# Kernel tuning notes

Measured on AMD Instinct MI355X. Metric: run time of the kernel, lower is better.

Reference implementation:

```python
import jax, jax.numpy as jnp
import numpy as np

T, B, C, H = 2048, 4, 1024, 16
DK = C // H
CLAMP = 1e8  # fp32 clamp bound used by the original module


def setup_inputs() -> dict:
    key = jax.random.key(0)
    ks = jax.random.split(key, 12)
    s = 1.0 / np.sqrt(C)
    inp = {
        'query': jax.random.normal(ks[0], (T, B, C), jnp.float32),
        'key': jax.random.normal(ks[1], (T, B, C), jnp.float32),
        'value': jax.random.normal(ks[2], (T, B, C), jnp.float32),
        'key_padding_mask': jax.random.randint(ks[3], (B, T), 0, 2) > 0,
        # nn.Linear params, stored torch-style as [out, in]
        'Wq': jax.random.uniform(ks[4], (C, C), jnp.float32, -s, s),
        'bq': jax.random.uniform(ks[5], (C,), jnp.float32, -s, s),
        'Wk': jax.random.uniform(ks[6], (C, C), jnp.float32, -s, s),
        'bk': jax.random.uniform(ks[7], (C,), jnp.float32, -s, s),
        'Wv': jax.random.uniform(ks[8], (C, C), jnp.float32, -s, s),
        'bv': jax.random.uniform(ks[9], (C,), jnp.float32, -s, s),
        'Wo': jax.random.uniform(ks[10], (C, C), jnp.float32, -s, s),
        'bo': jax.random.uniform(ks[11], (C,), jnp.float32, -s, s),
    }
    return inp


def _attn(query, key, value, key_padding_mask, Wq, bq, Wk, bk, Wv, bv, Wo, bo):
    # T x B x C -> B x T x C
    q_in = jnp.swapaxes(query, 0, 1)
    k_in = jnp.swapaxes(key, 0, 1)
    v_in = jnp.swapaxes(value, 0, 1)
    b = q_in.shape[0]
    # projections (torch Linear: x @ W.T + b), split heads -> B x H x T x dk
    q = (q_in @ Wq.T + bq).reshape(b, -1, H, DK).transpose(0, 2, 1, 3)
    k = (k_in @ Wk.T + bk).reshape(b, -1, H, DK).transpose(0, 2, 1, 3)
    v = (v_in @ Wv.T + bv).reshape(b, -1, H, DK).transpose(0, 2, 1, 3)
    scores = jnp.einsum('bhqd,bhkd->bhqk', q, k) / np.sqrt(DK)
    if key_padding_mask is not None:
        scores = jnp.where(key_padding_mask[:, None, None, :], -jnp.inf, scores)
    scores = jnp.clip(scores, -CLAMP, CLAMP)
    attn = jax.nn.softmax(scores.astype(jnp.float32), axis=-1).astype(scores.dtype)
    # dropout is identity in eval mode
    x = jnp.einsum('bhqk,bhkd->bhqd', attn, v)
    x = x.transpose(0, 2, 1, 3).reshape(b, -1, H * DK)
    out = x @ Wo.T + bo
    return jnp.swapaxes(out, 0, 1)  # back to T x B x C


def reference(query, key, value, key_padding_mask, Wq, bq, Wk, bk, Wv, bv, Wo, bo):
    return _attn(query, key, value, key_padding_mask, Wq, bq, Wk, bk, Wv, bv, Wo, bo)
```

## Files before the change

### kernel.cpp

```cpp
#include <hip/hip_runtime.h>
#include <hip/hip_bf16.h>
#include <cstddef>
#include <cstdint>

constexpr int T  = 2048;
constexpr int B  = 4;
constexpr int C  = 1024;
constexpr int H  = 16;
constexpr int DK = 64;
constexpr int M  = T * B;
constexpr int NT = T / 64;

typedef __attribute__((ext_vector_type(8))) short bf16x8;
typedef __attribute__((ext_vector_type(4))) float f32x4;
typedef __attribute__((ext_vector_type(4))) unsigned short u16x4;
typedef __attribute__((ext_vector_type(8))) unsigned short u16x8;

__device__ inline unsigned short f2bf(float f) {
    union { float f; uint32_t u; } v; v.f = f;
    uint32_t u = v.u + 0x7fff + ((v.u >> 16) & 1);
    return (unsigned short)(u >> 16);
}
__device__ inline float bf2f(unsigned short h) {
    union { uint32_t u; float f; } v; v.u = (uint32_t)h << 16;
    return v.f;
}
__device__ inline uint32_t cvtpk_bf16(float lo, float hi) {
    uint32_t r;
    asm("v_cvt_pk_bf16_f32 %0, %1, %2" : "=v"(r) : "v"(lo), "v"(hi));
    return r;
}
__device__ inline void cfence() { asm volatile("" ::: "memory"); }

__device__ inline void block_sync_lds() {
    __builtin_amdgcn_sched_barrier(0);
    asm volatile("s_waitcnt lgkmcnt(0)" ::: "memory");
    __builtin_amdgcn_sched_barrier(0);
    __builtin_amdgcn_s_barrier();
    __builtin_amdgcn_sched_barrier(0);
}

__device__ inline void gload_lds16(const void* g, void* l) {
    auto gp = reinterpret_cast<const __attribute__((address_space(1))) char*>(
        reinterpret_cast<uintptr_t>(g));
    auto lp = reinterpret_cast<__attribute__((address_space(3))) char*>(
        reinterpret_cast<uintptr_t>(l));
    __builtin_amdgcn_global_load_lds(gp, lp, 16, 0, 0);
}

__global__ __launch_bounds__(256) void convert_in(const float* __restrict__ q,
                                                  const float* __restrict__ k,
                                                  const float* __restrict__ v,
                                                  unsigned short* __restrict__ dq,
                                                  unsigned short* __restrict__ dk2,
                                                  unsigned short* __restrict__ dv) {
    const float* s; unsigned short* d;
    if (blockIdx.y == 0) { s = q; d = dq; }
    else if (blockIdx.y == 1) { s = k; d = dk2; }
    else { s = v; d = dv; }
    const size_t i = ((size_t)blockIdx.x * 256 + threadIdx.x) * 8;
    const float4 a = *(const float4*)(s + i);
    const float4 b = *(const float4*)(s + i + 4);
    u16x8 o;
    o[0] = f2bf(a.x); o[1] = f2bf(a.y); o[2] = f2bf(a.z); o[3] = f2bf(a.w);
    o[4] = f2bf(b.x); o[5] = f2bf(b.y); o[6] = f2bf(b.z); o[7] = f2bf(b.w);
    *(u16x8*)(d + i) = o;
}

__global__ __launch_bounds__(256) void convert_w(const float* __restrict__ wq,
                                                 const float* __restrict__ wk,
                                                 const float* __restrict__ wv,
                                                 unsigned short* __restrict__ dst) {
    const float* s = blockIdx.y == 0 ? wq : (blockIdx.y == 1 ? wk : wv);
    unsigned short* d = dst + (size_t)blockIdx.y * C * C;
    const size_t i = ((size_t)blockIdx.x * 256 + threadIdx.x) * 8;
    const float4 a = *(const float4*)(s + i);
    const float4 b = *(const float4*)(s + i + 4);
    u16x8 o;
    o[0] = f2bf(a.x); o[1] = f2bf(a.y); o[2] = f2bf(a.z); o[3] = f2bf(a.w);
    o[4] = f2bf(b.x); o[5] = f2bf(b.y); o[6] = f2bf(b.z); o[7] = f2bf(b.w);
    *(u16x8*)(d + i) = o;
}

__global__ __launch_bounds__(256) void convert_wo(const float* __restrict__ wo,
                                                  unsigned short* __restrict__ hi,
                                                  unsigned short* __restrict__ lo) {
    const size_t i = ((size_t)blockIdx.x * 256 + threadIdx.x) * 8;
#pragma unroll
    for (int j = 0; j < 8; j++) {
        const float x = wo[i + j];
        const unsigned short h = f2bf(x);
        hi[i + j] = h;
        lo[i + j] = f2bf(x - bf2f(h));
    }
}

__global__ __launch_bounds__(256) void qkv_gemm(
        const unsigned short* __restrict__ Aq,
        const unsigned short* __restrict__ Ak,
        const unsigned short* __restrict__ Av,
        const unsigned short* __restrict__ W,
        const float* __restrict__ bq, const float* __restrict__ bk,
        const float* __restrict__ bv,
        unsigned short* __restrict__ Qb, unsigned short* __restrict__ Kb,
        unsigned short* __restrict__ Vb) {
    __shared__ __align__(16) unsigned short As[128][32];
    __shared__ __align__(16) unsigned short Ws[128][32];

    const int tid = threadIdx.x;
    const int m0 = blockIdx.x * 128;
    const int n0 = blockIdx.y * 128;
    const int w = tid >> 6, lane = tid & 63;
    const int g = lane >> 4, c16 = lane & 15;
    const int wr = (w >> 1) * 64, wc = (w & 1) * 64;

    const int which = n0 >> 10;
    const unsigned short* A = which == 0 ? Aq : (which == 1 ? Ak : Av);

    f32x4 acc[4][4] = {};

    for (int k0 = 0; k0 < C; k0 += 32) {
        __syncthreads();
#pragma unroll
        for (int half = 0; half < 2; half++) {
            const int chunk = tid + half * 256;
            const int r = chunk >> 2, s = chunk & 3;
            gload_lds16(A + (size_t)(m0 + r) * C + k0 + s * 8,
                        (char*)&As[0][0] + chunk * 16);
            gload_lds16(W + (size_t)(n0 + r) * C + k0 + s * 8,
                        (char*)&Ws[0][0] + chunk * 16);
        }
        __syncthreads();

        bf16x8 af[4], bfr[4];
#pragma unroll
        for (int mf = 0; mf < 4; mf++)
            af[mf] = *(const bf16x8*)&As[wr + mf * 16 + c16][g * 8];
#pragma unroll
        for (int nf = 0; nf < 4; nf++)
            bfr[nf] = *(const bf16x8*)&Ws[wc + nf * 16 + c16][g * 8];
#pragma unroll
        for (int mf = 0; mf < 4; mf++)
#pragma unroll
            for (int nf = 0; nf < 4; nf++)
                acc[mf][nf] = __builtin_amdgcn_mfma_f32_16x16x32_bf16(
                    af[mf], bfr[nf], acc[mf][nf], 0, 0, 0);
    }

    unsigned short* dst = which == 0 ? Qb : (which == 1 ? Kb : Vb);
    const float* bias = which == 0 ? bq : (which == 1 ? bk : bv);
    const float scale = which == 0 ? 0.180336889f : 1.0f;

#pragma unroll
    for (int mf = 0; mf < 4; mf++) {
#pragma unroll
        for (int nf = 0; nf < 4; nf++) {
            const int n = n0 + wc + nf * 16 + c16;
            const int c = n & 1023;
            const int hh = c >> 6, dk = c & 63;
            const float bval = bias[c];
#pragma unroll
            for (int r = 0; r < 4; r++) {
                const int m = m0 + wr + mf * 16 + g * 4 + r;
                const int t = m >> 2, bb = m & 3;
                dst[((size_t)(bb * H + hh) * T + t) * DK + dk] =
                    f2bf((acc[mf][nf][r] + bval) * scale);
            }
        }
    }
}

__global__ __launch_bounds__(256) void oproj_gemm(
        const unsigned short* __restrict__ Xh, const unsigned short* __restrict__ Xl,
        const unsigned short* __restrict__ Wh, const unsigned short* __restrict__ Wl,
        const float* __restrict__ bo, float* __restrict__ out) {
    __shared__ __align__(16) unsigned short Ahs[128][32];
    __shared__ __align__(16) unsigned short Als[128][32];
    __shared__ __align__(16) unsigned short Bhs[128][32];
    __shared__ __align__(16) unsigned short Bls[128][32];

    const int tid = threadIdx.x;
    const int m0 = blockIdx.x * 128;
    const int n0 = blockIdx.y * 128;
    const int w = tid >> 6, lane = tid & 63;
    const int g = lane >> 4, c16 = lane & 15;
    const int wr = (w >> 1) * 64, wc = (w & 1) * 64;

    f32x4 acc[4][4] = {};

    for (int k0 = 0; k0 < C; k0 += 32) {
        __syncthreads();
#pragma unroll
        for (int half = 0; half < 2; half++) {
            const int chunk = tid + half * 256;
            const int r = chunk >> 2, s = chunk & 3;
            const size_t goffA = (size_t)(m0 + r) * C + k0 + s * 8;
            const size_t goffB = (size_t)(n0 + r) * C + k0 + s * 8;
            gload_lds16(Xh + goffA, (char*)&Ahs[0][0] + chunk * 16);
            gload_lds16(Xl + goffA, (char*)&Als[0][0] + chunk * 16);
            gload_lds16(Wh + goffB, (char*)&Bhs[0][0] + chunk * 16);
            gload_lds16(Wl + goffB, (char*)&Bls[0][0] + chunk * 16);
        }
        __syncthreads();

        bf16x8 ah[4], al[4];
#pragma unroll
        for (int mf = 0; mf < 4; mf++) {
            ah[mf] = *(const bf16x8*)&Ahs[wr + mf * 16 + c16][g * 8];
            al[mf] = *(const bf16x8*)&Als[wr + mf * 16 + c16][g * 8];
        }
#pragma unroll
        for (int nf = 0; nf < 4; nf++) {
            const bf16x8 wh = *(const bf16x8*)&Bhs[wc + nf * 16 + c16][g * 8];
            const bf16x8 wl = *(const bf16x8*)&Bls[wc + nf * 16 + c16][g * 8];
#pragma unroll
            for (int mf = 0; mf < 4; mf++) {
                acc[mf][nf] = __builtin_amdgcn_mfma_f32_16x16x32_bf16(ah[mf], wh, acc[mf][nf], 0, 0, 0);
                acc[mf][nf] = __builtin_amdgcn_mfma_f32_16x16x32_bf16(al[mf], wh, acc[mf][nf], 0, 0, 0);
                acc[mf][nf] = __builtin_amdgcn_mfma_f32_16x16x32_bf16(ah[mf], wl, acc[mf][nf], 0, 0, 0);
            }
        }
    }

#pragma unroll
    for (int mf = 0; mf < 4; mf++) {
#pragma unroll
        for (int nf = 0; nf < 4; nf++) {
            const int n = n0 + wc + nf * 16 + c16;
            const float bval = bo[n];
#pragma unroll
            for (int r = 0; r < 4; r++) {
                const int m = m0 + wr + mf * 16 + g * 4 + r;
                const int t = m & 2047, bb = m >> 11;
                out[((size_t)t * B + bb) * C + n] = acc[mf][nf][r] + bval;
            }
        }
    }
}

__global__ __launch_bounds__(256) void attn_mfma(const unsigned short* __restrict__ Q,
                                                 const unsigned short* __restrict__ K,
                                                 const unsigned short* __restrict__ V,
                                                 const int* __restrict__ mask,
                                                 unsigned short* __restrict__ Xh,
                                                 unsigned short* __restrict__ Xl) {
    __shared__ __align__(16) short Ks[2][64][72];
    __shared__ __align__(16) short Vt[2][64][72];
    __shared__ __align__(16) short Pl[4][16][72];

    const int b = blockIdx.z, h = blockIdx.y;
    const int q0 = blockIdx.x * 128;
    const int tid = threadIdx.x;
    const int wl = tid >> 6;
    const int lane = tid & 63;
    const int g = lane >> 4;
    const int c16 = lane & 15;

    const size_t bh = (size_t)(b * H + h) * T * DK;
    const unsigned short* Qg = Q + bh;
    const unsigned short* Kg = K + bh;
    const unsigned short* Vg = V + bh;
    const int* mb = mask + b * T;

    bf16x8 qf[2][2];
#pragma unroll
    for (int qs = 0; qs < 2; qs++)
#pragma unroll
        for (int sl = 0; sl < 2; sl++)
            qf[qs][sl] = *(const bf16x8*)(Qg +
                (size_t)(q0 + wl * 32 + qs * 16 + c16) * DK + g * 8 + sl * 32);

    f32x4 o[2][4] = {};
    float lrow[2] = {0.0f, 0.0f};

    const int skr = tid >> 3;
    const int skc = (tid & 7) * 8;
    const int kp = tid & 31, dc = tid >> 5;
    uint4 kra, krb; u16x8 va, vb; int mw;

#define ISSUE(kv0)                                                              \
    do {                                                                        \
        kra = *(const uint4*)(Kg + (size_t)((kv0) + skr) * DK + skc);           \
        krb = *(const uint4*)(Kg + (size_t)((kv0) + skr + 32) * DK + skc);      \
        va  = *(const u16x8*)(Vg + (size_t)((kv0) + 2 * kp) * DK + dc * 8);     \
        vb  = *(const u16x8*)(Vg + (size_t)((kv0) + 2 * kp + 1) * DK + dc * 8); \
        mw  = mb[(kv0) + lane];                                                 \
    } while (0)

    ISSUE(0);

    for (int kt = 0; kt < NT; ++kt) {
        const int buf = kt & 1;

        const unsigned long long mbits = __ballot(mw != 0);
        *(uint4*)&Ks[buf][skr][skc] = kra;
        *(uint4*)&Ks[buf][skr + 32][skc] = krb;
#pragma unroll
        for (int j = 0; j < 8; j++) {
            *(uint32_t*)&Vt[buf][dc * 8 + j][2 * kp] =
                (uint32_t)(unsigned short)va[j] | ((uint32_t)(unsigned short)vb[j] << 16);
        }
        if (kt + 1 < NT) ISSUE((kt + 1) * 64);

        block_sync_lds();

        bf16x8 kf[4][2], vf[4][2];
#pragma unroll
        for (int t = 0; t < 4; t++)
#pragma unroll
            for (int sl = 0; sl < 2; sl++) {
                kf[t][sl] = *(const bf16x8*)&Ks[buf][t * 16 + c16][g * 8 + sl * 32];
                vf[t][sl] = *(const bf16x8*)&Vt[buf][t * 16 + c16][g * 8 + sl * 32];
            }

#pragma unroll
        for (int qs = 0; qs < 2; qs++) {
            f32x4 s4[4];
#pragma unroll
            for (int t = 0; t < 4; t++) {
                f32x4 acc = {0.f, 0.f, 0.f, 0.f};
                acc = __builtin_amdgcn_mfma_f32_16x16x32_bf16(kf[t][0], qf[qs][0], acc, 0, 0, 0);
                acc = __builtin_amdgcn_mfma_f32_16x16x32_bf16(kf[t][1], qf[qs][1], acc, 0, 0, 0);
                s4[t] = acc;
            }

            float rs = 0.0f;
#pragma unroll
            for (int t = 0; t < 4; t++)
#pragma unroll
                for (int r = 0; r < 4; r++) {
                    float p = __builtin_amdgcn_exp2f(s4[t][r]);
                    const int key = 16 * t + 4 * g + r;
                    p = ((mbits >> key) & 1ull) ? 0.0f : p;
                    s4[t][r] = p;
                    rs += p;
                }
            rs += __shfl_xor(rs, 16);
            rs += __shfl_xor(rs, 32);
            lrow[qs] += rs;

            cfence();
#pragma unroll
            for (int t = 0; t < 4; t++)
#pragma unroll
                for (int rr = 0; rr < 2; rr++) {
                    const uint32_t wv = cvtpk_bf16(s4[t][2 * rr], s4[t][2 * rr + 1]);
                    *(uint32_t*)&Pl[wl][c16][16 * t + 4 * g + 2 * rr] = wv;
                }
            cfence();
            bf16x8 pa[2];
            pa[0] = *(const bf16x8*)&Pl[wl][c16][g * 8];
            pa[1] = *(const bf16x8*)&Pl[wl][c16][g * 8 + 32];
            cfence();

#pragma unroll
            for (int td = 0; td < 4; td++) {
                o[qs][td] = __builtin_amdgcn_mfma_f32_16x16x32_bf16(vf[td][0], pa[0], o[qs][td], 0, 0, 0);
                o[qs][td] = __builtin_amdgcn_mfma_f32_16x16x32_bf16(vf[td][1], pa[1], o[qs][td], 0, 0, 0);
            }
        }
    }
#undef ISSUE

#pragma unroll
    for (int qs = 0; qs < 2; qs++) {
        const float inv = 1.0f / lrow[qs];
        const int qq = q0 + wl * 32 + qs * 16 + c16;
#pragma unroll
        for (int td = 0; td < 4; td++) {
            u16x4 hi4, lo4;
#pragma unroll
            for (int r = 0; r < 4; r++) {
                const float val = o[qs][td][r] * inv;
                const unsigned short hv = f2bf(val);
                hi4[r] = hv;
                lo4[r] = f2bf(val - bf2f(hv));
            }
            const size_t idx = ((size_t)b * T + qq) * C + h * DK + td * 16 + 4 * g;
            *(u16x4*)(Xh + idx) = hi4;
            *(u16x4*)(Xl + idx) = lo4;
        }
    }
}

extern "C" void kernel_launch(void* const* d_in, const int* in_sizes, int n_in,
                              void* d_out, int out_size, void* d_ws, size_t ws_size,
                              hipStream_t stream) {
    const float* query = (const float*)d_in[0];
    const float* key   = (const float*)d_in[1];
    const float* value = (const float*)d_in[2];
    const int*   kpm   = (const int*)d_in[3];
    const float* Wq = (const float*)d_in[4];
    const float* bq = (const float*)d_in[5];
    const float* Wk = (const float*)d_in[6];
    const float* bk = (const float*)d_in[7];
    const float* Wv = (const float*)d_in[8];
    const float* bv = (const float*)d_in[9];
    const float* Wo = (const float*)d_in[10];
    const float* bo = (const float*)d_in[11];

    constexpr size_t MB = 1u << 20;
    char* w8 = (char*)d_ws;
    unsigned short* Qa  = (unsigned short*)(w8 + 0 * MB);
    unsigned short* Ka  = (unsigned short*)(w8 + 16 * MB);
    unsigned short* Va  = (unsigned short*)(w8 + 32 * MB);
    unsigned short* WB  = (unsigned short*)(w8 + 48 * MB);
    unsigned short* WoH = (unsigned short*)(w8 + 54 * MB);
    unsigned short* WoL = (unsigned short*)(w8 + 56 * MB);
    unsigned short* Qb  = (unsigned short*)(w8 + 64 * MB);
    unsigned short* Kb  = (unsigned short*)(w8 + 80 * MB);
    unsigned short* Vb  = (unsigned short*)(w8 + 96 * MB);
    unsigned short* XhB = Qa;
    unsigned short* XlB = Ka;

    const dim3 blk(256);

    convert_in<<<dim3(4096, 3), blk, 0, stream>>>(query, key, value, Qa, Ka, Va);
    convert_w<<<dim3(512, 3), blk, 0, stream>>>(Wq, Wk, Wv, WB);
    convert_wo<<<dim3(512, 1), blk, 0, stream>>>(Wo, WoH, WoL);

    qkv_gemm<<<dim3(M / 128, 3 * C / 128), blk, 0, stream>>>(Qa, Ka, Va, WB,
                                                             bq, bk, bv,
                                                             Qb, Kb, Vb);

    attn_mfma<<<dim3(T / 128, H, B), blk, 0, stream>>>(Qb, Kb, Vb, kpm, XhB, XlB);

    oproj_gemm<<<dim3(M / 128, C / 128), blk, 0, stream>>>(XhB, XlB, WoH, WoL,
                                                           bo, (float*)d_out);
}
```

Before: 273.1 us.

## Fuse input bf16 conversion into QKV GEMM and tune attention inner loop

```diff
diff --git a/kernel.cpp b/kernel.cpp
--- a/kernel.cpp
+++ b/kernel.cpp
@@ -46,25 +46,6 @@
     auto lp = reinterpret_cast<__attribute__((address_space(3))) char*>(
         reinterpret_cast<uintptr_t>(l));
     __builtin_amdgcn_global_load_lds(gp, lp, 16, 0, 0);
-}
-
-__global__ __launch_bounds__(256) void convert_in(const float* __restrict__ q,
-                                                  const float* __restrict__ k,
-                                                  const float* __restrict__ v,
-                                                  unsigned short* __restrict__ dq,
-                                                  unsigned short* __restrict__ dk2,
-                                                  unsigned short* __restrict__ dv) {
-    const float* s; unsigned short* d;
-    if (blockIdx.y == 0) { s = q; d = dq; }
-    else if (blockIdx.y == 1) { s = k; d = dk2; }
-    else { s = v; d = dv; }
-    const size_t i = ((size_t)blockIdx.x * 256 + threadIdx.x) * 8;
-    const float4 a = *(const float4*)(s + i);
-    const float4 b = *(const float4*)(s + i + 4);
-    u16x8 o;
-    o[0] = f2bf(a.x); o[1] = f2bf(a.y); o[2] = f2bf(a.z); o[3] = f2bf(a.w);
-    o[4] = f2bf(b.x); o[5] = f2bf(b.y); o[6] = f2bf(b.z); o[7] = f2bf(b.w);
-    *(u16x8*)(d + i) = o;
 }
 
 __global__ __launch_bounds__(256) void convert_w(const float* __restrict__ wq,
@@ -96,9 +77,9 @@
 }
 
 __global__ __launch_bounds__(256) void qkv_gemm(
-        const unsigned short* __restrict__ Aq,
-        const unsigned short* __restrict__ Ak,
-        const unsigned short* __restrict__ Av,
+        const float* __restrict__ Aq,
+        const float* __restrict__ Ak,
+        const float* __restrict__ Av,
         const unsigned short* __restrict__ W,
         const float* __restrict__ bq, const float* __restrict__ bk,
         const float* __restrict__ bv,
@@ -115,7 +96,10 @@
     const int wr = (w >> 1) * 64, wc = (w & 1) * 64;
 
     const int which = n0 >> 10;
-    const unsigned short* A = which == 0 ? Aq : (which == 1 ? Ak : Av);
+    const float* A = which == 0 ? Aq : (which == 1 ? Ak : Av);
+
+    const int ar = tid >> 1;
+    const int ab = (tid & 1) * 16;
 
     f32x4 acc[4][4] = {};
 
@@ -125,10 +109,22 @@
         for (int half = 0; half < 2; half++) {
             const int chunk = tid + half * 256;
             const int r = chunk >> 2, s = chunk & 3;
-            gload_lds16(A + (size_t)(m0 + r) * C + k0 + s * 8,
-                        (char*)&As[0][0] + chunk * 16);
             gload_lds16(W + (size_t)(n0 + r) * C + k0 + s * 8,
                         (char*)&Ws[0][0] + chunk * 16);
+        }
+        {
+            const float* Ap = A + (size_t)(m0 + ar) * C + k0 + ab;
+            const float4 a0 = *(const float4*)(Ap + 0);
+            const float4 a1 = *(const float4*)(Ap + 4);
+            const float4 a2 = *(const float4*)(Ap + 8);
+            const float4 a3 = *(const float4*)(Ap + 12);
+            uint4 w0, w1;
+            w0.x = cvtpk_bf16(a0.x, a0.y); w0.y = cvtpk_bf16(a0.z, a0.w);
+            w0.z = cvtpk_bf16(a1.x, a1.y); w0.w = cvtpk_bf16(a1.z, a1.w);
+            w1.x = cvtpk_bf16(a2.x, a2.y); w1.y = cvtpk_bf16(a2.z, a2.w);
+            w1.z = cvtpk_bf16(a3.x, a3.y); w1.w = cvtpk_bf16(a3.z, a3.w);
+            *(uint4*)&As[ar][ab] = w0;
+            *(uint4*)&As[ar][ab + 8] = w1;
         }
         __syncthreads();
 
@@ -304,6 +300,10 @@
 
         block_sync_lds();
 
+        const unsigned long long nib = mbits >> (4 * g);
+        const uint32_t nlo = (uint32_t)nib;
+        const uint32_t nhi = (uint32_t)(nib >> 32);
+
         bf16x8 kf[4][2], vf[4][2];
 #pragma unroll
         for (int t = 0; t < 4; t++)
@@ -316,6 +316,7 @@
 #pragma unroll
         for (int qs = 0; qs < 2; qs++) {
             f32x4 s4[4];
+            __builtin_amdgcn_s_setprio(1);
 #pragma unroll
             for (int t = 0; t < 4; t++) {
                 f32x4 acc = {0.f, 0.f, 0.f, 0.f};
@@ -323,21 +324,18 @@
                 acc = __builtin_amdgcn_mfma_f32_16x16x32_bf16(kf[t][1], qf[qs][1], acc, 0, 0, 0);
                 s4[t] = acc;
             }
-
-            float rs = 0.0f;
-#pragma unroll
-            for (int t = 0; t < 4; t++)
+            __builtin_amdgcn_s_setprio(0);
+
+#pragma unroll
+            for (int t = 0; t < 4; t++) {
+                const uint32_t sel = (t & 2) ? nhi : nlo;
 #pragma unroll
                 for (int r = 0; r < 4; r++) {
                     float p = __builtin_amdgcn_exp2f(s4[t][r]);
-                    const int key = 16 * t + 4 * g + r;
-                    p = ((mbits >> key) & 1ull) ? 0.0f : p;
+                    p = ((sel >> ((t & 1) * 16 + r)) & 1u) ? 0.0f : p;
                     s4[t][r] = p;
-                    rs += p;
                 }
-            rs += __shfl_xor(rs, 16);
-            rs += __shfl_xor(rs, 32);
-            lrow[qs] += rs;
+            }
 
             cfence();
 #pragma unroll
@@ -353,11 +351,22 @@
             pa[1] = *(const bf16x8*)&Pl[wl][c16][g * 8 + 32];
             cfence();
 
+            __builtin_amdgcn_s_setprio(1);
 #pragma unroll
             for (int td = 0; td < 4; td++) {
                 o[qs][td] = __builtin_amdgcn_mfma_f32_16x16x32_bf16(vf[td][0], pa[0], o[qs][td], 0, 0, 0);
                 o[qs][td] = __builtin_amdgcn_mfma_f32_16x16x32_bf16(vf[td][1], pa[1], o[qs][td], 0, 0, 0);
             }
+            __builtin_amdgcn_s_setprio(0);
+
+            float rs = 0.0f;
+#pragma unroll
+            for (int t = 0; t < 4; t++)
+#pragma unroll
+                for (int r = 0; r < 4; r++) rs += s4[t][r];
+            rs += __shfl_xor(rs, 16);
+            rs += __shfl_xor(rs, 32);
+            lrow[qs] += rs;
         }
     }
 #undef ISSUE
@@ -401,26 +410,22 @@
 
     constexpr size_t MB = 1u << 20;
     char* w8 = (char*)d_ws;
-    unsigned short* Qa  = (unsigned short*)(w8 + 0 * MB);
-    unsigned short* Ka  = (unsigned short*)(w8 + 16 * MB);
-    unsigned short* Va  = (unsigned short*)(w8 + 32 * MB);
+    unsigned short* XhB = (unsigned short*)(w8 + 0 * MB);
+    unsigned short* XlB = (unsigned short*)(w8 + 16 * MB);
     unsigned short* WB  = (unsigned short*)(w8 + 48 * MB);
     unsigned short* WoH = (unsigned short*)(w8 + 54 * MB);
     unsigned short* WoL = (unsigned short*)(w8 + 56 * MB);
     unsigned short* Qb  = (unsigned short*)(w8 + 64 * MB);
     unsigned short* Kb  = (unsigned short*)(w8 + 80 * MB);
     unsigned short* Vb  = (unsigned short*)(w8 + 96 * MB);
-    unsigned short* XhB = Qa;
-    unsigned short* XlB = Ka;
 
     const dim3 blk(256);
 
-    convert_in<<<dim3(4096, 3), blk, 0, stream>>>(query, key, value, Qa, Ka, Va);
     convert_w<<<dim3(512, 3), blk, 0, stream>>>(Wq, Wk, Wv, WB);
     convert_wo<<<dim3(512, 1), blk, 0, stream>>>(Wo, WoH, WoL);
 
-    qkv_gemm<<<dim3(M / 128, 3 * C / 128), blk, 0, stream>>>(Qa, Ka, Va, WB,
-                                                             bq, bk, bv,
+    qkv_gemm<<<dim3(M / 128, 3 * C / 128), blk, 0, stream>>>(query, key, value,
+                                                             WB, bq, bk, bv,
                                                              Qb, Kb, Vb);
 
     attn_mfma<<<dim3(T / 128, H, B), blk, 0, stream>>>(Qb, Kb, Vb, kpm, XhB, XlB);
```

Result: slower. 322.7 us (+18.2%).
